# Optimization experiments

Measured on AMD Instinct MI355X. Metric: run time of the kernel, lower is better.

The kernel has to match this reference:

```python
import jax, jax.numpy as jnp
import numpy as np

W, E, D, NL, NC = 2048, 256, 512, 4, 5
DI, DS, DR, DC = 1024, 64, 32, 4  # d_inner=2*D, d_state, dt_rank=ceil(D/16), d_conv


def setup_inputs() -> dict:
    key = jax.random.key(0)
    ks = jax.random.split(key, 24)
    s = 0.02
    byte_sequence = jax.random.randint(ks[0], (2, W), 0, 256, dtype=jnp.int32)
    p = {
        "byte_sequence": byte_sequence,
        "byte_embed": jax.random.normal(ks[1], (256, E)) * s,
        "pos_embed": jax.random.normal(ks[2], (W, E)) * s,
        "in_w": jax.random.normal(ks[3], (D, E)) * s,
        "in_b": jnp.zeros((D,)),
        "ln_g": jnp.ones((NL, D)),
        "ln_b": jnp.zeros((NL, D)),
        "m_in_w": jax.random.normal(ks[4], (NL, 2 * DI, D)) * s,
        "conv_w": jax.random.normal(ks[5], (NL, DI, DC)) * s,
        "conv_b": jnp.zeros((NL, DI)),
        "xp_w": jax.random.normal(ks[6], (NL, DR + 2 * DS, DI)) * s,
        "dt_w": jax.random.normal(ks[7], (NL, DI, DR)) * s,
        "dt_b": jnp.full((NL, DI), -4.6),  # softplus(-4.6) ~ 0.01, in [dt_min, dt_max]
        "A_log": jnp.broadcast_to(jnp.log(jnp.arange(1.0, DS + 1.0)), (NL, DI, DS)) + 0.0,
        "Dp": jnp.ones((NL, DI)),
        "m_out_w": jax.random.normal(ks[8], (NL, D, DI)) * s,
        "h1_w": jax.random.normal(ks[9], (256, D)) * s,
        "h1_b": jnp.zeros((256,)),
        "h2_w": jax.random.normal(ks[10], (128, 256)) * s,
        "h2_b": jnp.zeros((128,)),
        "h3_w": jax.random.normal(ks[11], (NC, 128)) * s,
        "h3_b": jnp.zeros((NC,)),
    }
    return p


def _layernorm(x, g, b, eps=1e-5):
    mu = jnp.mean(x, axis=-1, keepdims=True)
    var = jnp.mean((x - mu) ** 2, axis=-1, keepdims=True)
    return (x - mu) * jax.lax.rsqrt(var + eps) * g + b


def _mamba(x, in_w, cw, cb, xp_w, dt_w, dt_b, A_log, Dp_, out_w):
    B, L, _ = x.shape
    xr = x @ in_w.T                       # [B,L,2*DI]
    xs, res = xr[..., :DI], xr[..., DI:]
    # causal depthwise conv1d over L
    xc = jnp.transpose(xs, (0, 2, 1))     # [B,DI,L]
    xc = jax.lax.conv_general_dilated(xc, cw[:, None, :], (1,), [(DC - 1, 0)], feature_group_count=DI)
    xs = jax.nn.silu(jnp.transpose(xc + cb[None, :, None], (0, 2, 1)))  # [B,L,DI]
    xdbl = xs @ xp_w.T                    # [B,L,DR+2*DS]
    dt, Bm, Cm = xdbl[..., :DR], xdbl[..., DR:DR + DS], xdbl[..., DR + DS:]
    delta = jax.nn.softplus(dt @ dt_w.T + dt_b)  # [B,L,DI]
    A = -jnp.exp(A_log)                   # [DI,DS]

    def step(h, inp):
        d_t, B_t, C_t, x_t = inp          # [B,DI],[B,DS],[B,DS],[B,DI]
        dA = jnp.exp(d_t[:, :, None] * A)             # [B,DI,DS]
        h = dA * h + (d_t * x_t)[:, :, None] * B_t[:, None, :]
        y = jnp.einsum('bds,bs->bd', h, C_t)
        return h, y

    h0 = jnp.zeros((B, DI, DS), x.dtype)
    seq = (jnp.swapaxes(delta, 0, 1), jnp.swapaxes(Bm, 0, 1), jnp.swapaxes(Cm, 0, 1), jnp.swapaxes(xs, 0, 1))
    _, ys = jax.lax.scan(step, h0, seq)   # ys: [L,B,DI]
    y = jnp.swapaxes(ys, 0, 1) + xs * Dp_
    y = y * jax.nn.silu(res)
    return y @ out_w.T


def reference(byte_sequence, byte_embed, pos_embed, in_w, in_b, ln_g, ln_b, m_in_w, conv_w, conv_b, xp_w, dt_w, dt_b, A_log, Dp, m_out_w, h1_w, h1_b, h2_w, h2_b, h3_w, h3_b):
    B, L = byte_sequence.shape
    x = byte_embed[byte_sequence] + pos_embed[None, :L]  # [B,L,E]
    x = x @ in_w.T + in_b                                # [B,L,D]
    for i in range(NL):
        res = x
        h = _layernorm(x, ln_g[i], ln_b[i])
        h = _mamba(h, m_in_w[i], conv_w[i], conv_b[i], xp_w[i], dt_w[i], dt_b[i], A_log[i], Dp[i], m_out_w[i])
        x = h + res
    h = jax.nn.relu(x @ h1_w.T + h1_b)
    h = jax.nn.relu(h @ h2_w.T + h2_b)
    return h @ h3_w.T + h3_b
```

## Files before the change

kernel.cpp:

```cpp
#include <hip/hip_runtime.h>
#include <hip/hip_bf16.h>

#define WLEN 2048
#define EDIM 256
#define DDIM 512
#define NLAYER 4
#define NCLS 5
#define DI 1024
#define DS 64
#define DR 32
#define DC 4
#define BB 2
#define TOK (BB*WLEN)
#define XD (DR + 2*DS)
#define CL 128
#define NCH (WLEN/CL)
#define LOG2E 1.44269504f

typedef __bf16 bf16x8 __attribute__((ext_vector_type(8)));
typedef float  f32x4  __attribute__((ext_vector_type(4)));

static __device__ __forceinline__ unsigned short f2bf(float f) {
    union { float f; unsigned u; } v; v.f = f;
    unsigned r = v.u + 0x7fffu + ((v.u >> 16) & 1u);
    return (unsigned short)(r >> 16);
}

__global__ __launch_bounds__(256) void embed_k(const int* __restrict__ seq,
    const float* __restrict__ be, const float* __restrict__ pe,
    float* __restrict__ out)
{
    int idx = blockIdx.x * 256 + threadIdx.x;
    int e  = idx & (EDIM - 1);
    int bl = idx >> 8;
    int l  = bl & (WLEN - 1);
    int tok = seq[bl];
    out[idx] = be[tok * EDIM + e] + pe[l * EDIM + e];
}

__global__ __launch_bounds__(256) void ln_k(const float* __restrict__ x,
    const float* __restrict__ g, const float* __restrict__ b,
    unsigned short* __restrict__ out)
{
    int row  = blockIdx.x * 4 + (threadIdx.x >> 6);
    int lane = threadIdx.x & 63;
    const float* xp = x + (size_t)row * DDIM;
    float v[8];
    float s = 0.f;
#pragma unroll
    for (int i = 0; i < 8; i++) { v[i] = xp[lane + 64 * i]; s += v[i]; }
#pragma unroll
    for (int off = 32; off; off >>= 1) s += __shfl_xor(s, off, 64);
    float mu = s * (1.f / 512.f);
    float s2 = 0.f;
#pragma unroll
    for (int i = 0; i < 8; i++) { float d = v[i] - mu; s2 += d * d; }
#pragma unroll
    for (int off = 32; off; off >>= 1) s2 += __shfl_xor(s2, off, 64);
    float rs = rsqrtf(s2 * (1.f / 512.f) + 1e-5f);
#pragma unroll
    for (int i = 0; i < 8; i++) {
        int c = lane + 64 * i;
        out[(size_t)row * DDIM + c] = f2bf((v[i] - mu) * rs * g[c] + b[c]);
    }
}

__global__ __launch_bounds__(256) void conv_t_k(const float* __restrict__ xcT,
    const float* __restrict__ cw, const float* __restrict__ cb,
    float* __restrict__ xsT)
{
    int gid  = blockIdx.x * 256 + threadIdx.x;
    int row  = gid >> 9;
    int col0 = (gid & 511) << 3;
    int l0   = col0 & (WLEN - 1);
    const float* src = xcT + (size_t)row * TOK + col0;
    float xw[12];
    if (l0 > 0) {
        float4 a = *(const float4*)(src - 4);
        xw[0] = a.x; xw[1] = a.y; xw[2] = a.z; xw[3] = a.w;
    } else {
        xw[0] = xw[1] = xw[2] = xw[3] = 0.f;
    }
    float4 m0 = *(const float4*)src;
    float4 m1 = *(const float4*)(src + 4);
    xw[4] = m0.x; xw[5] = m0.y; xw[6] = m0.z; xw[7] = m0.w;
    xw[8] = m1.x; xw[9] = m1.y; xw[10] = m1.z; xw[11] = m1.w;
    float w0 = cw[row * DC + 0], w1 = cw[row * DC + 1];
    float w2 = cw[row * DC + 2], w3 = cw[row * DC + 3];
    float bias = cb[row];
    float o[8];
#pragma unroll
    for (int u = 0; u < 8; u++) {
        float a = bias;
        a = fmaf(w0, xw[u + 1], a);
        a = fmaf(w1, xw[u + 2], a);
        a = fmaf(w2, xw[u + 3], a);
        a = fmaf(w3, xw[u + 4], a);
        o[u] = a / (1.f + __expf(-a));
    }
    float* dst = xsT + (size_t)row * TOK + col0;
    *(float4*)dst       = make_float4(o[0], o[1], o[2], o[3]);
    *(float4*)(dst + 4) = make_float4(o[4], o[5], o[6], o[7]);
}

__global__ __launch_bounds__(256) void f2bf2_k(
    const float* __restrict__ in1, unsigned short* __restrict__ out1, int n1,
    const float* __restrict__ in2, unsigned short* __restrict__ out2, int n2)
{
    int i = blockIdx.x * 256 + threadIdx.x;
    if (i < n1) out1[i] = f2bf(in1[i]);
    else if (i < n1 + n2) out2[i - n1] = f2bf(in2[i - n1]);
}

__global__ __launch_bounds__(256) void trans_BC_k(const float* __restrict__ xdblT,
    float* __restrict__ BC)
{
    __shared__ float tile[64][65];
    int bt = blockIdx.x;
    int half = blockIdx.y;
    int col = threadIdx.x & 63, rr = threadIdx.x >> 6;
    int srow0 = DR + half * DS;
#pragma unroll
    for (int k = 0; k < 16; k++) {
        int i = k * 4 + rr;
        tile[i][col] = xdblT[(size_t)(srow0 + i) * TOK + bt * 64 + col];
    }
    __syncthreads();
#pragma unroll
    for (int k = 0; k < 16; k++) {
        int tt = k * 4 + rr;
        BC[(size_t)(bt * 64 + tt) * 128 + half * 64 + col] = tile[col][tt];
    }
}

__global__ __launch_bounds__(256) void trans_y_k(const unsigned short* __restrict__ yT,
    unsigned short* __restrict__ ybf)
{
    __shared__ unsigned short tile[64][72];
    int bt = blockIdx.x, bd = blockIdx.y, b = blockIdx.z;
    int col = threadIdx.x & 63, rr = threadIdx.x >> 6;
#pragma unroll
    for (int k = 0; k < 16; k++) {
        int i = k * 4 + rr;
        tile[i][col] = yT[(size_t)(bd * 64 + i) * TOK + b * WLEN + bt * 64 + col];
    }
    __syncthreads();
#pragma unroll
    for (int k = 0; k < 16; k++) {
        int tt = k * 4 + rr;
        ybf[((size_t)(b * WLEN + bt * 64 + tt)) * DI + bd * 64 + col] = tile[col][tt];
    }
}

#define SU 8

#define LOADG1(T0, dlt, xv, Bt, Ct)                                      \
  {                                                                      \
    *(float4*)&dlt[0] = *(const float4*)&dRow[(T0)];                     \
    *(float4*)&dlt[4] = *(const float4*)&dRow[(T0) + 4];                 \
    *(float4*)&xv[0]  = *(const float4*)&xRow[(T0)];                     \
    *(float4*)&xv[4]  = *(const float4*)&xRow[(T0) + 4];                 \
    const float* bc = BCrow + (size_t)(T0) * 128 + lane;                 \
    _Pragma("unroll")                                                    \
    for (int u = 0; u < SU; u++) {                                       \
      Bt[u] = bc[u * 128];                                               \
      Ct[u] = bc[u * 128 + 64];                                          \
    }                                                                    \
  }

#define COMPG1(T0, dlt, xv, Bt, Ct)                                      \
  {                                                                      \
    float dA[SU], p[SU], cds[SU];                                        \
    _Pragma("unroll")                                                    \
    for (int u = 0; u < SU; u++) dA[u] = __expf(dlt[u] * Aa);            \
    _Pragma("unroll")                                                    \
    for (int u = 0; u < SU; u++) {                                       \
      hst = fmaf(dA[u], hst, dlt[u] * xv[u] * Bt[u]);                    \
      p[u] = fmaf(xv[u], Dp0, hst * Ct[u]);                              \
    }                                                                    \
    cds[0] = cd + dlt[0];                                                \
    _Pragma("unroll")                                                    \
    for (int u = 1; u < SU; u++) cds[u] = cds[u - 1] + dlt[u];           \
    cd = cds[SU - 1];                                                    \
    if (lane == 0) {                                                     \
      *(float4*)&cdRow[(T0)]     = make_float4(cds[0], cds[1], cds[2], cds[3]); \
      *(float4*)&cdRow[(T0) + 4] = make_float4(cds[4], cds[5], cds[6], cds[7]); \
    }                                                                    \
    _Pragma("unroll")                                                    \
    for (int u = 0; u < SU; u++) wred[u * 64 + lane] = p[u];             \
    float4 q0 = *(const float4*)&wred[(lane >> 3) * 64 + (lane & 7) * 8];     \
    float4 q1 = *(const float4*)&wred[(lane >> 3) * 64 + (lane & 7) * 8 + 4]; \
    float sred = ((q0.x + q0.y) + (q0.z + q0.w)) +                       \
                 ((q1.x + q1.y) + (q1.z + q1.w));                        \
    sred += __shfl_xor(sred, 1, 64);                                     \
    sred += __shfl_xor(sred, 2, 64);                                     \
    sred += __shfl_xor(sred, 4, 64);                                     \
    if ((lane & 7) == 0) zRow[(T0) + (lane >> 3)] = sred;                \
  }

__global__ __launch_bounds__(256) void scan1_k(
    const float* __restrict__ deltaT,
    const float* __restrict__ BC,
    const float* __restrict__ xsT,
    const float* __restrict__ A_log,
    const float* __restrict__ Dp,
    float* __restrict__ zT,
    float* __restrict__ cdT,
    float* __restrict__ Hbuf,
    float* __restrict__ Sbuf)
{
    __shared__ float red[4 * SU * 64];
    int wv   = threadIdx.x >> 6;
    float* wred = red + wv * (SU * 64);
    int wid  = blockIdx.x * 4 + wv;
    int lane = threadIdx.x & 63;
    int c  = wid & (NCH - 1);
    int bd = wid >> 4;
    int d  = bd & (DI - 1);
    int b  = bd >> 10;
    size_t col0 = (size_t)b * WLEN + (size_t)c * CL;
    const float* dRow  = deltaT + (size_t)d * TOK + col0;
    const float* xRow  = xsT    + (size_t)d * TOK + col0;
    const float* BCrow = BC + col0 * 128;
    float* zRow  = zT  + (size_t)d * TOK + col0;
    float* cdRow = cdT + (size_t)d * TOK + col0;
    float Aa  = -__expf(A_log[d * DS + lane]);
    float Dp0 = (lane == 0) ? Dp[d] : 0.f;
    float hst = 0.f, cd = 0.f;

    float da[SU], xa[SU], Ba[SU], Ca[SU];
    float db[SU], xb[SU], Bb[SU], Cb[SU];

    LOADG1(0, da, xa, Ba, Ca)
    for (int t0 = 0; t0 < CL; t0 += 2 * SU) {
        LOADG1(t0 + SU, db, xb, Bb, Cb)
        COMPG1(t0, da, xa, Ba, Ca)
        if (t0 + 2 * SU < CL)
            LOADG1(t0 + 2 * SU, da, xa, Ba, Ca)
        COMPG1(t0 + SU, db, xb, Bb, Cb)
    }
    Hbuf[(size_t)wid * DS + lane] = hst;
    if (lane == 0) Sbuf[wid] = cd;
}

__global__ __launch_bounds__(256) void scan2_k(
    const float* __restrict__ Hbuf, const float* __restrict__ Sbuf,
    const float* __restrict__ A_log, float* __restrict__ h0buf)
{
    int bd   = blockIdx.x * 4 + (threadIdx.x >> 6);
    int lane = threadIdx.x & 63;
    int d = bd & (DI - 1);
    float Aa = -__expf(A_log[d * DS + lane]);
    float h = 0.f;
#pragma unroll
    for (int c = 0; c < NCH; c++) {
        size_t i = (size_t)bd * NCH + c;
        h0buf[i * DS + lane] = h;
        h = __expf(Aa * Sbuf[i]) * h + Hbuf[i * DS + lane];
    }
}

static __device__ __forceinline__ float lanef(float v, int s) {
    return __uint_as_float(__builtin_amdgcn_readlane(__float_as_uint(v), s));
}

__global__ __launch_bounds__(256) void scan3_k(
    const float* __restrict__ zT,
    const float* __restrict__ cdT,
    const float* __restrict__ rT,
    const float* __restrict__ xdblT,
    const float* __restrict__ A_log,
    const float* __restrict__ h0buf,
    unsigned short* __restrict__ yT)
{
    int wid  = blockIdx.x * 4 + (threadIdx.x >> 6);
    int lane = threadIdx.x & 63;
    int c  = wid & (NCH - 1);
    int bd = wid >> 4;
    int d  = bd & (DI - 1);
    int b  = bd >> 10;
    float Kv  = -__expf(A_log[d * DS + lane]) * LOG2E;
    float h0v = h0buf[(size_t)wid * DS + lane];
    size_t rowb = (size_t)d * TOK + (size_t)b * WLEN;
    const float* Cb = xdblT + (size_t)(DR + DS) * TOK + (size_t)b * WLEN;

#pragma unroll
    for (int pass = 0; pass < CL / 64; pass++) {
        int t = c * CL + pass * 64 + lane;
        float cd = cdT[rowb + t];
        float z  = zT[rowb + t];
        float r  = rT[rowb + t];
        float c0 = 0.f, c1 = 0.f, c2 = 0.f, c3 = 0.f;
#pragma unroll
        for (int s = 0; s < DS; s += 4) {
            float C0 = Cb[(size_t)(s + 0) * TOK + t];
            float C1 = Cb[(size_t)(s + 1) * TOK + t];
            float C2 = Cb[(size_t)(s + 2) * TOK + t];
            float C3 = Cb[(size_t)(s + 3) * TOK + t];
            c0 = fmaf(C0 * lanef(h0v, s + 0), exp2f(lanef(Kv, s + 0) * cd), c0);
            c1 = fmaf(C1 * lanef(h0v, s + 1), exp2f(lanef(Kv, s + 1) * cd), c1);
            c2 = fmaf(C2 * lanef(h0v, s + 2), exp2f(lanef(Kv, s + 2) * cd), c2);
            c3 = fmaf(C3 * lanef(h0v, s + 3), exp2f(lanef(Kv, s + 3) * cd), c3);
        }
        float corr = (c0 + c1) + (c2 + c3);
        float yv = (z + corr) * (r / (1.f + __expf(-r)));
        yT[rowb + t] = f2bf(yv);
    }
}

template<int EPI>
__global__ __launch_bounds__(256) void gemm_bf16(
    const unsigned short* __restrict__ A,
    const unsigned short* __restrict__ W,
    const float* __restrict__ resid,
    float* __restrict__ C,
    float* __restrict__ T0buf,
    float* __restrict__ T1buf,
    int M, int N, int K)
{
    __shared__ unsigned short As[4 * 128 * 8];
    __shared__ unsigned short Bs[4 * 128 * 8];
    const int tid = threadIdx.x;
    const int bm = blockIdx.x * 128, bn = blockIdx.y * 128;
    const int l = tid & 63, w = tid >> 6;
    const int wm = (w >> 1) * 64, wn = (w & 1) * 64;
    const int srow = tid >> 1, shalf = tid & 1;
    const int kq = l >> 4, lr = l & 15;

    f32x4 acc[4][4];
#pragma unroll
    for (int i = 0; i < 4; i++)
#pragma unroll
        for (int j = 0; j < 4; j++)
            acc[i][j] = f32x4{0.f, 0.f, 0.f, 0.f};

    for (int k0 = 0; k0 < K; k0 += 32) {
        const uint4* ga = (const uint4*)(A + (size_t)(bm + srow) * K + k0 + shalf * 16);
        uint4 a0 = ga[0], a1 = ga[1];
        const uint4* gb = (const uint4*)(W + (size_t)(bn + srow) * K + k0 + shalf * 16);
        uint4 b0 = gb[0], b1 = gb[1];
        __syncthreads();
        int kg = shalf * 2;
        *(uint4*)&As[((kg    ) * 128 + srow) * 8] = a0;
        *(uint4*)&As[((kg + 1) * 128 + srow) * 8] = a1;
        *(uint4*)&Bs[((kg    ) * 128 + srow) * 8] = b0;
        *(uint4*)&Bs[((kg + 1) * 128 + srow) * 8] = b1;
        __syncthreads();
        bf16x8 av[4], bv[4];
#pragma unroll
        for (int mf = 0; mf < 4; mf++)
            av[mf] = *(const bf16x8*)&As[(kq * 128 + wm + mf * 16 + lr) * 8];
#pragma unroll
        for (int nf = 0; nf < 4; nf++)
            bv[nf] = *(const bf16x8*)&Bs[(kq * 128 + wn + nf * 16 + lr) * 8];
#pragma unroll
        for (int mf = 0; mf < 4; mf++)
#pragma unroll
            for (int nf = 0; nf < 4; nf++)
                acc[mf][nf] = __builtin_amdgcn_mfma_f32_16x16x32_bf16(
                    av[mf], bv[nf], acc[mf][nf], 0, 0, 0);
    }
#pragma unroll
    for (int mf = 0; mf < 4; mf++) {
#pragma unroll
        for (int nf = 0; nf < 4; nf++) {
            int n  = bn + wn + nf * 16 + lr;
            int m0 = bm + wm + mf * 16 + kq * 4;
            if (EPI == 5) {
                float4 val = make_float4(acc[mf][nf][0], acc[mf][nf][1],
                                         acc[mf][nf][2], acc[mf][nf][3]);
                float* dst = (n < DI) ? &T0buf[(size_t)n * TOK + m0]
                                      : &T1buf[(size_t)(n - DI) * TOK + m0];
                *(float4*)dst = val;
            } else {
#pragma unroll
                for (int r = 0; r < 4; r++) {
                    int m = m0 + r;
                    float v = acc[mf][nf][r];
                    if (EPI == 4) v += resid[(size_t)m * N + n];
                    C[(size_t)m * N + n] = v;
                }
            }
        }
    }
}

template<int EPI>
__global__ __launch_bounds__(256) void gemm_nn(
    const float* __restrict__ A,
    const float* __restrict__ B,
    const float* __restrict__ bias,
    float* __restrict__ C,
    int M, int N, int K)
{
    __shared__ float As[16][64];
    __shared__ float Bs[16][64];
    const int tid = threadIdx.x;
    const int tx = tid & 15, ty = tid >> 4;
    const int bm = blockIdx.x * 64, bn = blockIdx.y * 64;
    const int arow = tid >> 2, ak = (tid & 3) << 2;
    const int brow = tid & 15, bn4 = (tid >> 4) << 2;
    float acc[4][4] = {};
    for (int k0 = 0; k0 < K; k0 += 16) {
        float4 av = make_float4(0.f, 0.f, 0.f, 0.f);
        if (bm + arow < M)
            av = *(const float4*)&A[(size_t)(bm + arow) * K + k0 + ak];
        float4 bv = *(const float4*)&B[(size_t)(k0 + brow) * N + bn + bn4];
        __syncthreads();
        As[ak + 0][arow] = av.x; As[ak + 1][arow] = av.y;
        As[ak + 2][arow] = av.z; As[ak + 3][arow] = av.w;
        *(float4*)&Bs[brow][bn4] = bv;
        __syncthreads();
#pragma unroll
        for (int k = 0; k < 16; ++k) {
            float4 a = *(const float4*)&As[k][ty * 4];
            float4 w = *(const float4*)&Bs[k][tx * 4];
            float aa[4] = {a.x, a.y, a.z, a.w};
            float ww[4] = {w.x, w.y, w.z, w.w};
#pragma unroll
            for (int i = 0; i < 4; i++)
#pragma unroll
                for (int j = 0; j < 4; j++)
                    acc[i][j] = fmaf(aa[i], ww[j], acc[i][j]);
        }
        __syncthreads();
    }
#pragma unroll
    for (int i = 0; i < 4; i++) {
        int m = bm + ty * 4 + i;
        if (m >= M) continue;
        float vv[4];
#pragma unroll
        for (int j = 0; j < 4; j++) {
            float v = acc[i][j];
            if (EPI == 3) {
                v += bias[m];
                v = fmaxf(v, 0.f) + log1pf(__expf(-fabsf(v)));
            }
            vv[j] = v;
        }
        *(float4*)&C[(size_t)m * N + bn + tx * 4] = make_float4(vv[0], vv[1], vv[2], vv[3]);
    }
}

template<int EPI>
__global__ __launch_bounds__(256) void gemm_nt(
    const float* __restrict__ A, int lda,
    const float* __restrict__ W, int ldw,
    const float* __restrict__ bias,
    float* __restrict__ C, int ldc,
    int M, int N, int K)
{
    __shared__ float As[16][64];
    __shared__ float Ws[16][64];
    const int tid = threadIdx.x;
    const int tx = tid & 15;
    const int ty = tid >> 4;
    const int bm = blockIdx.x * 64;
    const int bn = blockIdx.y * 64;
    const int lr = tid >> 2;
    const int lc = (tid & 3) << 2;
    float acc[4][4] = {};
    for (int k0 = 0; k0 < K; k0 += 16) {
        float4 av = *(const float4*)(A + (size_t)(bm + lr) * lda + (k0 + lc));
        float4 wv = make_float4(0.f, 0.f, 0.f, 0.f);
        if (bn + lr < N)
            wv = *(const float4*)(W + (size_t)(bn + lr) * ldw + (k0 + lc));
        As[lc + 0][lr] = av.x; As[lc + 1][lr] = av.y;
        As[lc + 2][lr] = av.z; As[lc + 3][lr] = av.w;
        Ws[lc + 0][lr] = wv.x; Ws[lc + 1][lr] = wv.y;
        Ws[lc + 2][lr] = wv.z; Ws[lc + 3][lr] = wv.w;
        __syncthreads();
#pragma unroll
        for (int k = 0; k < 16; ++k) {
            float4 a = *(const float4*)&As[k][ty * 4];
            float4 w = *(const float4*)&Ws[k][tx * 4];
            float aa[4] = {a.x, a.y, a.z, a.w};
            float ww[4] = {w.x, w.y, w.z, w.w};
#pragma unroll
            for (int i = 0; i < 4; i++)
#pragma unroll
                for (int j = 0; j < 4; j++)
                    acc[i][j] = fmaf(aa[i], ww[j], acc[i][j]);
        }
        __syncthreads();
    }
#pragma unroll
    for (int i = 0; i < 4; i++) {
        int m = bm + ty * 4 + i;
#pragma unroll
        for (int j = 0; j < 4; j++) {
            int n = bn + tx * 4 + j;
            if (n >= N) continue;
            float v = acc[i][j];
            v += bias[n];
            if (EPI == 2) v = fmaxf(v, 0.f);
            C[(size_t)m * ldc + n] = v;
        }
    }
}

extern "C" void kernel_launch(void* const* d_in, const int* in_sizes, int n_in,
                              void* d_out, int out_size, void* d_ws, size_t ws_size,
                              hipStream_t stream)
{
    const int*   seq        = (const int*)d_in[0];
    const float* byte_embed = (const float*)d_in[1];
    const float* pos_embed  = (const float*)d_in[2];
    const float* in_w       = (const float*)d_in[3];
    const float* in_b       = (const float*)d_in[4];
    const float* ln_g       = (const float*)d_in[5];
    const float* ln_b       = (const float*)d_in[6];
    const float* m_in_w     = (const float*)d_in[7];
    const float* conv_w     = (const float*)d_in[8];
    const float* conv_b     = (const float*)d_in[9];
    const float* xp_w       = (const float*)d_in[10];
    const float* dt_w       = (const float*)d_in[11];
    const float* dt_b       = (const float*)d_in[12];
    const float* A_log      = (const float*)d_in[13];
    const float* Dp         = (const float*)d_in[14];
    const float* m_out_w    = (const float*)d_in[15];
    const float* h1_w       = (const float*)d_in[16];
    const float* h1_b       = (const float*)d_in[17];
    const float* h2_w       = (const float*)d_in[18];
    const float* h2_b       = (const float*)d_in[19];
    const float* h3_w       = (const float*)d_in[20];
    const float* h3_b       = (const float*)d_in[21];
    float* out = (float*)d_out;

    float* ws = (float*)d_ws;
    size_t off = 0;
    float* xe     = ws + off; off += (size_t)TOK * EDIM;
    float* x      = ws + off; off += (size_t)TOK * DDIM;
    float* xcT    = ws + off; off += (size_t)DI * TOK;
    float* xsT    = ws + off; off += (size_t)DI * TOK;
    float* xdblT  = ws + off; off += (size_t)XD * TOK;
    float* BC     = ws + off; off += (size_t)TOK * 2 * DS;
    float* deltaT = ws + off; off += (size_t)DI * TOK;
    float* zT     = ws + off; off += (size_t)DI * TOK;
    float* cdT    = ws + off; off += (size_t)DI * TOK;
    float* rT     = ws + off; off += (size_t)DI * TOK;
    float* Hbuf   = ws + off; off += (size_t)BB * DI * NCH * DS;
    float* h0buf  = ws + off; off += (size_t)BB * DI * NCH * DS;
    float* Sbuf   = ws + off; off += (size_t)BB * DI * NCH;
    unsigned short* h_bf   = (unsigned short*)(ws + off); off += (size_t)TOK * DDIM / 2;
    unsigned short* y_bf   = (unsigned short*)(ws + off); off += (size_t)TOK * DI / 2;
    unsigned short* wmi_bf = (unsigned short*)(ws + off); off += (size_t)NLAYER * 2 * DI * DDIM / 2;
    unsigned short* wmo_bf = (unsigned short*)(ws + off); off += (size_t)NLAYER * DDIM * DI / 2;
    unsigned short* yT_bf = (unsigned short*)deltaT;
    float* t1 = xe;
    float* t2 = (float*)h_bf;

    {
        int n1 = NLAYER * 2 * DI * DDIM;
        int n2 = NLAYER * DDIM * DI;
        f2bf2_k<<<(n1 + n2 + 255) / 256, 256, 0, stream>>>(
            m_in_w, wmi_bf, n1, m_out_w, wmo_bf, n2);
    }

    embed_k<<<TOK * EDIM / 256, 256, 0, stream>>>(seq, byte_embed, pos_embed, xe);
    gemm_nt<1><<<dim3(TOK/64, DDIM/64), 256, 0, stream>>>(
        xe, EDIM, in_w, EDIM, in_b, x, DDIM, TOK, DDIM, EDIM);

    for (int i = 0; i < NLAYER; i++) {
        const float* lg  = ln_g  + (size_t)i * DDIM;
        const float* lb  = ln_b  + (size_t)i * DDIM;
        const unsigned short* miw = wmi_bf + (size_t)i * 2 * DI * DDIM;
        const float* cw  = conv_w + (size_t)i * DI * DC;
        const float* cb  = conv_b + (size_t)i * DI;
        const float* xpw = xp_w  + (size_t)i * XD * DI;
        const float* dtw = dt_w  + (size_t)i * DI * DR;
        const float* dtb = dt_b  + (size_t)i * DI;
        const float* al  = A_log + (size_t)i * DI * DS;
        const float* dp  = Dp    + (size_t)i * DI;
        const unsigned short* mow = wmo_bf + (size_t)i * DDIM * DI;

        ln_k<<<TOK/4, 256, 0, stream>>>(x, lg, lb, h_bf);
        gemm_bf16<5><<<dim3(TOK/128, 2*DI/128), 256, 0, stream>>>(
            h_bf, miw, nullptr, nullptr, xcT, rT, TOK, 2*DI, DDIM);
        conv_t_k<<<(DI * TOK / 8) / 256, 256, 0, stream>>>(xcT, cw, cb, xsT);
        gemm_nn<0><<<dim3((XD + 63) / 64, TOK / 64), 256, 0, stream>>>(
            xpw, xsT, nullptr, xdblT, XD, TOK, DI);
        trans_BC_k<<<dim3(TOK/64, 2), 256, 0, stream>>>(xdblT, BC);
        gemm_nn<3><<<dim3(DI / 64, TOK / 64), 256, 0, stream>>>(
            dtw, xdblT, dtb, deltaT, DI, TOK, DR);

        scan1_k<<<(BB*DI*NCH)/4, 256, 0, stream>>>(
            deltaT, BC, xsT, al, dp, zT, cdT, Hbuf, Sbuf);
        scan2_k<<<(BB*DI)/4, 256, 0, stream>>>(Hbuf, Sbuf, al, h0buf);
        scan3_k<<<(BB*DI*NCH)/4, 256, 0, stream>>>(
            zT, cdT, rT, xdblT, al, h0buf, yT_bf);
        trans_y_k<<<dim3(WLEN/64, DI/64, BB), 256, 0, stream>>>(yT_bf, y_bf);

        gemm_bf16<4><<<dim3(TOK/128, DDIM/128), 256, 0, stream>>>(
            y_bf, mow, x, x, nullptr, nullptr, TOK, DDIM, DI);
    }

    gemm_nt<2><<<dim3(TOK/64, 256/64), 256, 0, stream>>>(
        x, DDIM, h1_w, DDIM, h1_b, t1, 256, TOK, 256, DDIM);
    gemm_nt<2><<<dim3(TOK/64, 2), 256, 0, stream>>>(
        t1, 256, h2_w, 256, h2_b, t2, 128, TOK, 128, 256);
    gemm_nt<1><<<dim3(TOK/64, 1), 256, 0, stream>>>(
        t2, 128, h3_w, 128, h3_b, out, NCLS, TOK, NCLS, 128);
}
```

Baseline: 1.907 ms.

## Fuse B/C transpose into x-proj GEMM epilogue and stage B/C in LDS for scan

```diff
diff --git a/kernel.cpp b/kernel.cpp
--- a/kernel.cpp
+++ b/kernel.cpp
@@ -112,27 +112,6 @@
     else if (i < n1 + n2) out2[i - n1] = f2bf(in2[i - n1]);
 }
 
-__global__ __launch_bounds__(256) void trans_BC_k(const float* __restrict__ xdblT,
-    float* __restrict__ BC)
-{
-    __shared__ float tile[64][65];
-    int bt = blockIdx.x;
-    int half = blockIdx.y;
-    int col = threadIdx.x & 63, rr = threadIdx.x >> 6;
-    int srow0 = DR + half * DS;
-#pragma unroll
-    for (int k = 0; k < 16; k++) {
-        int i = k * 4 + rr;
-        tile[i][col] = xdblT[(size_t)(srow0 + i) * TOK + bt * 64 + col];
-    }
-    __syncthreads();
-#pragma unroll
-    for (int k = 0; k < 16; k++) {
-        int tt = k * 4 + rr;
-        BC[(size_t)(bt * 64 + tt) * 128 + half * 64 + col] = tile[col][tt];
-    }
-}
-
 __global__ __launch_bounds__(256) void trans_y_k(const unsigned short* __restrict__ yT,
     unsigned short* __restrict__ ybf)
 {
@@ -154,22 +133,23 @@
 
 #define SU 8
 
-#define LOADG1(T0, dlt, xv, Bt, Ct)                                      \
+#define LOADDX(T0, dlt, xv)                                              \
   {                                                                      \
     *(float4*)&dlt[0] = *(const float4*)&dRow[(T0)];                     \
     *(float4*)&dlt[4] = *(const float4*)&dRow[(T0) + 4];                 \
     *(float4*)&xv[0]  = *(const float4*)&xRow[(T0)];                     \
     *(float4*)&xv[4]  = *(const float4*)&xRow[(T0) + 4];                 \
-    const float* bc = BCrow + (size_t)(T0) * 128 + lane;                 \
+  }
+
+#define COMPG1(T0, dlt, xv)                                              \
+  {                                                                      \
+    const float* bl = &bcs[((T0) & 63) * 128 + lane];                    \
+    float Bt[SU], Ct[SU];                                                \
     _Pragma("unroll")                                                    \
     for (int u = 0; u < SU; u++) {                                       \
-      Bt[u] = bc[u * 128];                                               \
-      Ct[u] = bc[u * 128 + 64];                                          \
+      Bt[u] = bl[u * 128];                                               \
+      Ct[u] = bl[u * 128 + 64];                                          \
     }                                                                    \
-  }
-
-#define COMPG1(T0, dlt, xv, Bt, Ct)                                      \
-  {                                                                      \
     float dA[SU], p[SU], cds[SU];                                        \
     _Pragma("unroll")                                                    \
     for (int u = 0; u < SU; u++) dA[u] = __expf(dlt[u] * Aa);            \
@@ -209,35 +189,46 @@
     float* __restrict__ Hbuf,
     float* __restrict__ Sbuf)
 {
+    __shared__ float bcs[64 * 128];
     __shared__ float red[4 * SU * 64];
-    int wv   = threadIdx.x >> 6;
+    const int tid  = threadIdx.x;
+    const int wv   = tid >> 6;
+    const int lane = tid & 63;
     float* wred = red + wv * (SU * 64);
-    int wid  = blockIdx.x * 4 + wv;
-    int lane = threadIdx.x & 63;
-    int c  = wid & (NCH - 1);
-    int bd = wid >> 4;
+    int c  = blockIdx.x & (NCH - 1);
+    int bd = (blockIdx.x >> 4) * 4 + wv;
     int d  = bd & (DI - 1);
     int b  = bd >> 10;
+    int wid = (bd << 4) + c;
     size_t col0 = (size_t)b * WLEN + (size_t)c * CL;
     const float* dRow  = deltaT + (size_t)d * TOK + col0;
     const float* xRow  = xsT    + (size_t)d * TOK + col0;
-    const float* BCrow = BC + col0 * 128;
+    const float4* BCg  = (const float4*)(BC + col0 * 128);
     float* zRow  = zT  + (size_t)d * TOK + col0;
     float* cdRow = cdT + (size_t)d * TOK + col0;
     float Aa  = -__expf(A_log[d * DS + lane]);
     float Dp0 = (lane == 0) ? Dp[d] : 0.f;
     float hst = 0.f, cd = 0.f;
 
-    float da[SU], xa[SU], Ba[SU], Ca[SU];
-    float db[SU], xb[SU], Bb[SU], Cb[SU];
-
-    LOADG1(0, da, xa, Ba, Ca)
-    for (int t0 = 0; t0 < CL; t0 += 2 * SU) {
-        LOADG1(t0 + SU, db, xb, Bb, Cb)
-        COMPG1(t0, da, xa, Ba, Ca)
-        if (t0 + 2 * SU < CL)
-            LOADG1(t0 + 2 * SU, da, xa, Ba, Ca)
-        COMPG1(t0 + SU, db, xb, Bb, Cb)
+    float da[SU], xa[SU];
+    float db[SU], xb[SU];
+
+#pragma unroll
+    for (int half = 0; half < 2; half++) {
+        if (half) __syncthreads();
+#pragma unroll
+        for (int k = 0; k < 8; k++)
+            ((float4*)bcs)[k * 256 + tid] = BCg[half * 2048 + k * 256 + tid];
+        __syncthreads();
+        int base = half * 64;
+        LOADDX(base, da, xa)
+        for (int t0 = base; t0 < base + 64; t0 += 2 * SU) {
+            LOADDX(t0 + SU, db, xb)
+            COMPG1(t0, da, xa)
+            if (t0 + 2 * SU < base + 64)
+                LOADDX(t0 + 2 * SU, da, xa)
+            COMPG1(t0 + SU, db, xb)
+        }
     }
     Hbuf[(size_t)wid * DS + lane] = hst;
     if (lane == 0) Sbuf[wid] = cd;
@@ -391,6 +382,7 @@
     const float* __restrict__ B,
     const float* __restrict__ bias,
     float* __restrict__ C,
+    float* __restrict__ BCout,
     int M, int N, int K)
 {
     __shared__ float As[16][64];
@@ -440,6 +432,11 @@
             vv[j] = v;
         }
         *(float4*)&C[(size_t)m * N + bn + tx * 4] = make_float4(vv[0], vv[1], vv[2], vv[3]);
+        if (EPI == 5 && m >= DR) {
+#pragma unroll
+            for (int j = 0; j < 4; j++)
+                BCout[(size_t)(bn + tx * 4 + j) * 128 + (m - DR)] = vv[j];
+        }
     }
 }
 
@@ -579,11 +576,10 @@
         gemm_bf16<5><<<dim3(TOK/128, 2*DI/128), 256, 0, stream>>>(
             h_bf, miw, nullptr, nullptr, xcT, rT, TOK, 2*DI, DDIM);
         conv_t_k<<<(DI * TOK / 8) / 256, 256, 0, stream>>>(xcT, cw, cb, xsT);
-        gemm_nn<0><<<dim3((XD + 63) / 64, TOK / 64), 256, 0, stream>>>(
-            xpw, xsT, nullptr, xdblT, XD, TOK, DI);
-        trans_BC_k<<<dim3(TOK/64, 2), 256, 0, stream>>>(xdblT, BC);
+        gemm_nn<5><<<dim3((XD + 63) / 64, TOK / 64), 256, 0, stream>>>(
+            xpw, xsT, nullptr, xdblT, BC, XD, TOK, DI);
         gemm_nn<3><<<dim3(DI / 64, TOK / 64), 256, 0, stream>>>(
-            dtw, xdblT, dtb, deltaT, DI, TOK, DR);
+            dtw, xdblT, dtb, deltaT, nullptr, DI, TOK, DR);
 
         scan1_k<<<(BB*DI*NCH)/4, 256, 0, stream>>>(
             deltaT, BC, xsT, al, dp, zT, cdT, Hbuf, Sbuf);
```

Result: faster. 1.776 ms (-6.8%).
